# Kernel optimization log

Measured on AMD Instinct MI355X. Metric: run time of the kernel, lower is better.

## Reference

```python
import jax, jax.numpy as jnp
import numpy as np

N = 64
DX = np.pi / N
# torch.fft.fftfreq(N+1, d) == np.fft.fftfreq(N+1) / d ; d varies per env so keep base freqs
BASE_FREQ = (2.0 * np.pi * np.fft.fftfreq(N + 1)).astype(np.float32)  # [65]
DOMAIN = np.array([0.75, 1.0, 0.75, 1.0, 0.75, 1.0, 0.75, 1.0], dtype=np.float32)


def _poisson_solve(w, dx_b):
    # w: [B,N,N] vorticity (already negated), dx_b: [B]
    w_pad = jnp.pad(w, ((0, 0), (0, 1), (0, 1)), mode='wrap')          # circular pad (0,1,0,1) -> [B,65,65]
    wf = jnp.fft.fft2(w_pad / (N ** 2))
    f = BASE_FREQ[None, :] / dx_b[:, None]                             # [B,65] per-env wavenumbers
    k2 = f[:, :, None] ** 2 + f[:, None, :] ** 2                       # [B,65,65] (meshgrid 'ij': kxx^2+kyy^2)
    uf = -wf / (1e-12 + k2)
    uf = uf.at[:, 0, 0].set(0.0)
    return jnp.fft.ifft2((N ** 2) * uf).real[:, :N, :N]                # [B,N,N]


def reference(t, y0, env, params):
    x = y0[:, 0]                                                       # [B,N,N]
    env = env.astype(jnp.int32)
    mu = params[env, 0][:, None, None]                                 # [B,1,1]
    fdx = (jnp.asarray(DOMAIN)[env] * DX)[:, None, None]               # [B,1,1]

    psi = _poisson_solve(-x, fdx[:, 0, 0])

    dxp = lambda a: jnp.roll(a, -1, axis=2) - jnp.roll(a, 1, axis=2)   # derive_x
    dyp = lambda a: jnp.roll(a, -1, axis=1) - jnp.roll(a, 1, axis=1)   # derive_y
    inv4 = 1.0 / (4.0 * fdx ** 2)

    J1 = (dyp(psi) * dxp(x) - dxp(psi) * dyp(x)) * inv4
    J2 = (jnp.roll(x, -1, axis=2) * dyp(jnp.roll(psi, -1, axis=2))
          - jnp.roll(x, 1, axis=2) * dyp(jnp.roll(psi, 1, axis=2))
          - jnp.roll(x, -1, axis=1) * dxp(jnp.roll(psi, -1, axis=1))
          + jnp.roll(x, 1, axis=1) * dxp(jnp.roll(psi, 1, axis=1))) * inv4
    J3 = (jnp.roll(x, (-1, -1), axis=(1, 2)) * (jnp.roll(psi, -1, axis=1) - jnp.roll(psi, -1, axis=2))
          - jnp.roll(x, (1, 1), axis=(1, 2)) * (jnp.roll(psi, 1, axis=2) - jnp.roll(psi, 1, axis=1))
          - jnp.roll(x, (-1, 1), axis=(1, 2)) * (jnp.roll(psi, -1, axis=1) - jnp.roll(psi, 1, axis=2))
          + jnp.roll(x, (1, -1), axis=(1, 2)) * (jnp.roll(psi, -1, axis=2) - jnp.roll(psi, 1, axis=1))) * inv4

    # circular-pad conv2d with kernel [[0,1,0],[1,-4,1],[1,1,0]] == cross-correlation stencil below
    lap = (jnp.roll(x, 1, axis=1) + jnp.roll(x, -1, axis=1)
           + jnp.roll(x, 1, axis=2) + jnp.roll(x, -1, axis=2)
           + jnp.roll(x, (-1, 1), axis=(1, 2)) - 4.0 * x) / (fdx ** 2)

    dudt = -(J1 + J2 + J3) / 3.0 + mu * lap
    return dudt[:, None]                                               # [B,1,N,N]


def setup_inputs() -> dict:
    key = jax.random.key(0)
    k1, k2 = jax.random.split(key)
    B, n_env = 2048, 8
    y0 = jax.random.normal(k1, (B, 1, N, N), dtype=jnp.float32)
    env = jax.random.randint(k2, (B,), 0, n_env, dtype=jnp.int64)
    params = jnp.concatenate([jnp.full((n_env, 1), 0.005, jnp.float32),
                              jnp.full((n_env, 1), 1.0, jnp.float32)], axis=1)
    t = jnp.zeros((1,), dtype=jnp.float32)
    return {"t": t, "y0": y0, "env": env, "params": params}
```

## Files before the change

kernel.cpp:

```cpp
#include <hip/hip_runtime.h>
#include <hip/hip_bf16.h>
#include <math.h>

#define P65 65
#define PLANE_U16 5248
#define SIDE_OFF  5120
#define PSI_U16   8320

__device__ __align__(16) ushort gAfrag[18*512];
__device__ float  g_MpPad[65*68];
__device__ float  g64tab[65];

__device__ __constant__ float c_DOMAIN[8] = {0.75f,1.0f,0.75f,1.0f,0.75f,1.0f,0.75f,1.0f};

__device__ inline ushort f2bf(float f) {
  return __bfloat16_as_ushort(__float2bfloat16(f));
}
__device__ inline float bf2f(ushort h) { return __uint_as_float(((unsigned)h) << 16); }

__device__ inline void barrier_lds() {
  asm volatile("s_waitcnt lgkmcnt(0)" ::: "memory");
  __builtin_amdgcn_sched_barrier(0);
  __builtin_amdgcn_s_barrier();
  __builtin_amdgcn_sched_barrier(0);
}

__device__ inline float Gvalf(int r, int i) {
  int m = (r <= 32) ? r : (r - 32);
  int prod = (m * (i % 65)) % 65;
  float ang = 6.2831853071795864769f * (float)prod / 65.0f;
  return (r <= 32) ? cosf(ang) : sinf(ang);
}
__device__ inline float Gfoldf(int r, int i) {
  float v = Gvalf(r, i);
  if (i == 0) v += Gvalf(r, 64);
  return v;
}

__global__ void init_tables() {
  int tid = blockIdx.x*blockDim.x + threadIdx.x;
  int nth = gridDim.x*blockDim.x;
  for (int idx = tid; idx < 18*512; idx += nth) {
    int blk = idx >> 9, rem = idx & 511;
    int lane = rem >> 3, e = rem & 7;
    int i16 = lane & 15, kg = lane >> 4;
    float v = 0.f;
    if (blk < 10) {
      int mt = blk >> 1, kt = blk & 1;
      int r = 16*mt + i16;
      int i = 32*kt + 8*kg + e;
      if (r < 65 && i < 64) v = Gfoldf(r, i);
    } else {
      int b2 = blk - 10;
      int mt = b2 >> 1, kt = b2 & 1;
      int j  = 16*mt + i16;
      int k1 = 32*kt + 8*kg + e;
      if (j < 64 && k1 < 64) v = Gvalf(k1, j);
    }
    gAfrag[idx] = f2bf(v);
  }
  for (int idx = tid; idx < 65*68; idx += nth) {
    int k2 = idx/68, k1 = idx%68;
    float v = 0.f;
    if (k1 <= 64 && (k1 | k2)) {
      float n1 = (k1==0)?(1.0f/65.0f):(2.0f/65.0f);
      float n2 = (k2==0)?(1.0f/65.0f):(2.0f/65.0f);
      int m1 = (k1<=32)?k1:(k1-32), m2 = (k2<=32)?k2:(k2-32);
      float b1 = 6.2831853071795864769f*(float)m1/65.0f;
      float b2 = 6.2831853071795864769f*(float)m2/65.0f;
      v = (n1*n2)/(b1*b1 + b2*b2);
    }
    g_MpPad[idx] = v;
  }
  for (int idx = tid; idx < 65; idx += nth)
    g64tab[idx] = (idx < 64) ? Gvalf(64, idx) : 0.f;
}

typedef __attribute__((ext_vector_type(8))) short bf16x8;
typedef __attribute__((ext_vector_type(4))) float f32x4;

template<int JT, int TBLOFF>
__device__ inline void prefetchA(bf16x8 (&pre)[2][2], int wvu, int lane, int NTL) {
  #pragma unroll
  for (int tb = 0; tb < 2; ++tb) {
    int tile = wvu + 8*tb;
    int tl = (tile < NTL) ? tile : 0;
    int jt = tl % JT;
    #pragma unroll
    for (int kt = 0; kt < 2; ++kt)
      pre[tb][kt] = *(const bf16x8*)(gAfrag + (TBLOFF + jt*2 + kt)*512 + lane*8);
  }
}

template<int IT, int JT, int TBLOFF, bool SCALE, bool RK, bool PSI>
__device__ inline void stage(const bf16x8 (&pre)[2][2],
                             const ushort* __restrict__ Lin,
                             ushort* __restrict__ Lout,
                             float* __restrict__ psiout,
                             int wvu, int lane)
{
  const int lg = lane >> 4, li = lane & 15;
  constexpr int NTL = IT*JT;
  constexpr int TPW = (NTL + 7) >> 3;
  #pragma unroll
  for (int tb = 0; tb < TPW; ++tb) {
    const int tile = wvu + 8*tb;
    if (tile >= NTL) continue;
    const int it = tile / JT, jt = tile - it*JT;
    f32x4 acc = {0.f, 0.f, 0.f, 0.f};
    #pragma unroll
    for (int kt = 0; kt < 2; ++kt) {
      bf16x8 af = (tb < 2) ? pre[tb][kt]
                           : *(const bf16x8*)(gAfrag + (TBLOFF + jt*2 + kt)*512 + lane*8);
      bf16x8 df = *(const bf16x8*)(Lin + (it*2 + kt)*512 + lane*8);
      acc = __builtin_amdgcn_mfma_f32_16x16x32_bf16(df, af, acc, 0, 0, 0);
    }
    const int f     = 16*jt + li;
    const int dbase = 16*it + 4*lg;
    const bool dEdge = (IT == 5) && (it == IT-1);
    const bool fEdge = (JT == 5) && (jt == JT-1);

    float v[4];
    #pragma unroll
    for (int r = 0; r < 4; ++r) v[r] = acc[r];

    if (SCALE) {
      const float* mp = g_MpPad + (fEdge ? 64 : f)*68 + (dEdge ? 64 : dbase);
      if (dEdge) v[0] *= mp[0];
      else {
        f32x4 m4 = *(const f32x4*)mp;
        #pragma unroll
        for (int r = 0; r < 4; ++r) v[r] *= m4[r];
      }
    }
    if (RK) {
      float gv = g64tab[f];
      uint2 sc = *(const uint2*)(Lin + SIDE_OFF + dbase);
      v[0] = fmaf(bf2f((ushort)(sc.x      )), gv, v[0]);
      v[1] = fmaf(bf2f((ushort)(sc.x >> 16)), gv, v[1]);
      v[2] = fmaf(bf2f((ushort)(sc.y      )), gv, v[2]);
      v[3] = fmaf(bf2f((ushort)(sc.y >> 16)), gv, v[3]);
    }

    if (PSI) {
      #pragma unroll
      for (int r = 0; r < 4; ++r) psiout[f*65 + dbase + r] = v[r];
    } else if (dEdge) {
      if (lg == 0 && (!fEdge || li == 0))
        Lout[SIDE_OFF + f] = f2bf(v[0]);
    } else {
      if (!fEdge || li == 0) {
        int wb = (2*jt + (it>>1))*512 + ((2*it + (lg>>1))&3)*128 + li*8 + 4*(lg&1);
        uint2 pk;
        pk.x = ((unsigned)f2bf(v[1]) << 16) | (unsigned)f2bf(v[0]);
        pk.y = ((unsigned)f2bf(v[3]) << 16) | (unsigned)f2bf(v[2]);
        *(uint2*)(Lout + wb) = pk;
      }
    }
  }
}

__device__ inline float shflx(float v, int srclane) { return __shfl(v, srclane, 64); }

__global__ void __launch_bounds__(512) pde_main(const float* __restrict__ y0,
                                                const int*   __restrict__ env,
                                                const float* __restrict__ params,
                                                float*       __restrict__ out)
{
  __shared__ __align__(16) ushort Lsh[PLANE_U16 + PSI_U16];
  ushort* PB   = Lsh;
  ushort* PA   = Lsh + PLANE_U16;
  float*  Ppsi = (float*)(Lsh + PLANE_U16);

  const int b    = blockIdx.x;
  const int t    = threadIdx.x;
  const int lane = t & 63;
  const int wvu  = __builtin_amdgcn_readfirstlane(t >> 6);

  const int   e       = env[b];
  const float mu      = params[2*e];
  const float fdx     = c_DOMAIN[e] * (float)(3.14159265358979323846/64.0);
  const float inv_dx2 = 1.0f/(fdx*fdx);

  const float* xb = y0 + (size_t)b*4096;

  const int j0 = wvu*8, jm0 = (j0+63)&63, jp8 = (j0+8)&63;
  float xbm = xb[jm0*64 + lane];
  float xbp = xb[jp8*64 + lane];

  float xr[8];
  bf16x8 hv;
  #pragma unroll
  for (int k=0;k<8;++k) {
    float v = xb[(8*wvu + k)*64 + lane];
    xr[k] = v;
    hv[k] = (short)f2bf(v);
  }
  {
    int wb = ((lane>>4)*2 + (wvu>>2))*512 + ((wvu&3)*16 + (lane&15))*8;
    *(bf16x8*)(PA + wb) = hv;
  }
  bf16x8 p1[2][2];  prefetchA<5,0>(p1, wvu, lane, 20);
  barrier_lds();

  stage<4,5, 0,false,false,false>(p1, PA, PB, nullptr, wvu, lane);
  bf16x8 p2[2][2];  prefetchA<5,0>(p2, wvu, lane, 25);
  barrier_lds();

  stage<5,5, 0,true ,false,false>(p2, PB, PA, nullptr, wvu, lane);
  bf16x8 p3[2][2];  prefetchA<4,10>(p3, wvu, lane, 20);
  barrier_lds();

  stage<5,4,10,false,true ,false>(p3, PA, PB, nullptr, wvu, lane);
  bf16x8 p4[2][2];  prefetchA<4,10>(p4, wvu, lane, 16);
  barrier_lds();

  stage<4,4,10,false,true ,true >(p4, PB, nullptr, Ppsi, wvu, lane);
  barrier_lds();

  {
    const int c = lane, cm = (c+63)&63, cp = (c+1)&63;
    const int cB = c*65, cmB = cm*65, cpB = cp*65;
    float* op = out + (size_t)b*4096;

    float xm_c = xbm,   xm_m = shflx(xm_c, cm), xm_p = shflx(xm_c, cp);
    float xc_c = xr[0], xc_m = shflx(xc_c, cm), xc_p = shflx(xc_c, cp);
    float pm_m = Ppsi[cmB+jm0], pm_c = Ppsi[cB+jm0], pm_p = Ppsi[cpB+jm0];
    float pc_m = Ppsi[cmB+j0 ], pc_c = Ppsi[cB+j0 ], pc_p = Ppsi[cpB+j0 ];

    #pragma unroll
    for (int m=0;m<8;++m) {
      int j = j0 + m, jp = (j+1)&63;
      float xn_c = (m < 7) ? xr[m+1] : xbp;
      float xn_m = shflx(xn_c, cm), xn_p = shflx(xn_c, cp);
      float pn_m = Ppsi[cmB+jp], pn_c = Ppsi[cB+jp], pn_p = Ppsi[cpB+jp];

      float J1 = (pn_c - pm_c)*(xc_p - xc_m) - (pc_p - pc_m)*(xn_c - xm_c);
      float J2 = xc_p*(pn_p - pm_p) - xc_m*(pn_m - pm_m)
               - xn_c*(pn_p - pn_m) + xm_c*(pm_p - pm_m);
      float J3 = xn_p*(pn_c - pc_p) - xm_m*(pc_m - pm_c)
               - xn_m*(pn_c - pc_m) + xm_p*(pc_p - pm_c);
      float lap = (xm_c + xn_c + xc_m + xc_p + xn_m - 4.0f*xc_c) * inv_dx2;

      op[j*64 + c] = -(J1 + J2 + J3)*(0.25f/3.0f) + mu*lap;

      xm_m=xc_m; xm_c=xc_c; xm_p=xc_p;  pm_m=pc_m; pm_c=pc_c; pm_p=pc_p;
      xc_m=xn_m; xc_c=xn_c; xc_p=xn_p;  pc_m=pn_m; pc_c=pn_c; pc_p=pn_p;
    }
  }
}

extern "C" void kernel_launch(void* const* d_in, const int* in_sizes, int n_in,
                              void* d_out, int out_size, void* d_ws, size_t ws_size,
                              hipStream_t stream) {
  const float* y0     = (const float*)d_in[1];
  const int*   env    = (const int*)  d_in[2];
  const float* params = (const float*)d_in[3];
  float*       out    = (float*)d_out;
  int B = in_sizes[1] / 4096;

  init_tables<<<64, 256, 0, stream>>>();
  pde_main<<<B, 512, 0, stream>>>(y0, env, params, out);
}
```

Before: 34.54 us.

## Process two images per block, sharing prefetched DFT fragments across both

Each workgroup now handles two batch images instead of one, with LDS doubled to hold both planes. The prefetched A-matrix fragments for each transform stage are reused for both images, and each stage is issued twice per barrier, halving the number of blocks and barriers per image. The cost is double the LDS and more register pressure per block, which may lower occupancy, and half as many blocks to spread across CUs.

```diff
diff --git a/kernel.cpp b/kernel.cpp
--- a/kernel.cpp
+++ b/kernel.cpp
@@ -6,6 +6,7 @@
 #define PLANE_U16 5248
 #define SIDE_OFF  5120
 #define PSI_U16   8320
+#define IMG_U16   (PLANE_U16 + PSI_U16)
 
 __device__ __align__(16) ushort gAfrag[18*512];
 __device__ float  g_MpPad[65*68];
@@ -162,92 +163,118 @@
 
 __device__ inline float shflx(float v, int srclane) { return __shfl(v, srclane, 64); }
 
+__device__ inline void stencil_img(const float* __restrict__ Ppsi,
+                                   const float* __restrict__ xr,
+                                   float xbm, float xbp,
+                                   float mu, float id2,
+                                   float* __restrict__ op,
+                                   int wvu, int lane, bool store)
+{
+  const int c = lane, cm = (c+63)&63, cp = (c+1)&63;
+  const int cB = c*65, cmB = cm*65, cpB = cp*65;
+  const int j0 = wvu*8, jm0 = (j0+63)&63;
+
+  float xm_c = xbm,   xm_m = shflx(xm_c, cm), xm_p = shflx(xm_c, cp);
+  float xc_c = xr[0], xc_m = shflx(xc_c, cm), xc_p = shflx(xc_c, cp);
+  float pm_m = Ppsi[cmB+jm0], pm_c = Ppsi[cB+jm0], pm_p = Ppsi[cpB+jm0];
+  float pc_m = Ppsi[cmB+j0 ], pc_c = Ppsi[cB+j0 ], pc_p = Ppsi[cpB+j0 ];
+
+  #pragma unroll
+  for (int m=0;m<8;++m) {
+    int j = j0 + m, jp = (j+1)&63;
+    float xn_c = (m < 7) ? xr[m+1] : xbp;
+    float xn_m = shflx(xn_c, cm), xn_p = shflx(xn_c, cp);
+    float pn_m = Ppsi[cmB+jp], pn_c = Ppsi[cB+jp], pn_p = Ppsi[cpB+jp];
+
+    float J1 = (pn_c - pm_c)*(xc_p - xc_m) - (pc_p - pc_m)*(xn_c - xm_c);
+    float J2 = xc_p*(pn_p - pm_p) - xc_m*(pn_m - pm_m)
+             - xn_c*(pn_p - pn_m) + xm_c*(pm_p - pm_m);
+    float J3 = xn_p*(pn_c - pc_p) - xm_m*(pc_m - pm_c)
+             - xn_m*(pn_c - pc_m) + xm_p*(pc_p - pm_c);
+    float lap = (xm_c + xn_c + xc_m + xc_p + xn_m - 4.0f*xc_c) * id2;
+
+    if (store) op[j*64 + c] = -(J1 + J2 + J3)*(0.25f/3.0f) + mu*lap;
+
+    xm_m=xc_m; xm_c=xc_c; xm_p=xc_p;  pm_m=pc_m; pm_c=pc_c; pm_p=pc_p;
+    xc_m=xn_m; xc_c=xn_c; xc_p=xn_p;  pc_m=pn_m; pc_c=pn_c; pc_p=pn_p;
+  }
+}
+
 __global__ void __launch_bounds__(512) pde_main(const float* __restrict__ y0,
                                                 const int*   __restrict__ env,
                                                 const float* __restrict__ params,
-                                                float*       __restrict__ out)
+                                                float*       __restrict__ out,
+                                                int B)
 {
-  __shared__ __align__(16) ushort Lsh[PLANE_U16 + PSI_U16];
-  ushort* PB   = Lsh;
-  ushort* PA   = Lsh + PLANE_U16;
-  float*  Ppsi = (float*)(Lsh + PLANE_U16);
-
-  const int b    = blockIdx.x;
+  __shared__ __align__(16) ushort Lsh[2*IMG_U16];
+  ushort* PB0 = Lsh;
+  ushort* PA0 = Lsh + PLANE_U16;
+  float*  Ps0 = (float*)(Lsh + PLANE_U16);
+  ushort* PB1 = Lsh + IMG_U16;
+  ushort* PA1 = Lsh + IMG_U16 + PLANE_U16;
+  float*  Ps1 = (float*)(Lsh + IMG_U16 + PLANE_U16);
+
   const int t    = threadIdx.x;
   const int lane = t & 63;
   const int wvu  = __builtin_amdgcn_readfirstlane(t >> 6);
 
-  const int   e       = env[b];
-  const float mu      = params[2*e];
-  const float fdx     = c_DOMAIN[e] * (float)(3.14159265358979323846/64.0);
-  const float inv_dx2 = 1.0f/(fdx*fdx);
-
-  const float* xb = y0 + (size_t)b*4096;
+  const int b0  = 2*blockIdx.x;
+  const int b1r = b0 + 1;
+  const bool has2 = (b1r < B);
+  const int b1 = has2 ? b1r : b0;
+
+  const int   e0 = env[b0], e1 = env[b1];
+  const float mu0 = params[2*e0], mu1 = params[2*e1];
+  const float fdx0 = c_DOMAIN[e0] * (float)(3.14159265358979323846/64.0);
+  const float fdx1 = c_DOMAIN[e1] * (float)(3.14159265358979323846/64.0);
+  const float id20 = 1.0f/(fdx0*fdx0);
+  const float id21 = 1.0f/(fdx1*fdx1);
+
+  const float* xb0 = y0 + (size_t)b0*4096;
+  const float* xb1 = y0 + (size_t)b1*4096;
 
   const int j0 = wvu*8, jm0 = (j0+63)&63, jp8 = (j0+8)&63;
-  float xbm = xb[jm0*64 + lane];
-  float xbp = xb[jp8*64 + lane];
-
-  float xr[8];
-  bf16x8 hv;
-  #pragma unroll
-  for (int k=0;k<8;++k) {
-    float v = xb[(8*wvu + k)*64 + lane];
-    xr[k] = v;
-    hv[k] = (short)f2bf(v);
-  }
+  float xbm0 = xb0[jm0*64 + lane], xbp0 = xb0[jp8*64 + lane];
+  float xbm1 = xb1[jm0*64 + lane], xbp1 = xb1[jp8*64 + lane];
+
+  float xr0[8], xr1[8];
   {
+    bf16x8 h0, h1;
+    #pragma unroll
+    for (int k=0;k<8;++k) {
+      float v0 = xb0[(8*wvu + k)*64 + lane];
+      float v1 = xb1[(8*wvu + k)*64 + lane];
+      xr0[k] = v0;  h0[k] = (short)f2bf(v0);
+      xr1[k] = v1;  h1[k] = (short)f2bf(v1);
+    }
     int wb = ((lane>>4)*2 + (wvu>>2))*512 + ((wvu&3)*16 + (lane&15))*8;
-    *(bf16x8*)(PA + wb) = hv;
+    *(bf16x8*)(PA0 + wb) = h0;
+    *(bf16x8*)(PA1 + wb) = h1;
   }
   bf16x8 p1[2][2];  prefetchA<5,0>(p1, wvu, lane, 20);
   barrier_lds();
 
-  stage<4,5, 0,false,false,false>(p1, PA, PB, nullptr, wvu, lane);
+  stage<4,5, 0,false,false,false>(p1, PA0, PB0, nullptr, wvu, lane);
+  stage<4,5, 0,false,false,false>(p1, PA1, PB1, nullptr, wvu, lane);
   bf16x8 p2[2][2];  prefetchA<5,0>(p2, wvu, lane, 25);
   barrier_lds();
 
-  stage<5,5, 0,true ,false,false>(p2, PB, PA, nullptr, wvu, lane);
+  stage<5,5, 0,true ,false,false>(p2, PB0, PA0, nullptr, wvu, lane);
+  stage<5,5, 0,true ,false,false>(p2, PB1, PA1, nullptr, wvu, lane);
   bf16x8 p3[2][2];  prefetchA<4,10>(p3, wvu, lane, 20);
   barrier_lds();
 
-  stage<5,4,10,false,true ,false>(p3, PA, PB, nullptr, wvu, lane);
+  stage<5,4,10,false,true ,false>(p3, PA0, PB0, nullptr, wvu, lane);
+  stage<5,4,10,false,true ,false>(p3, PA1, PB1, nullptr, wvu, lane);
   bf16x8 p4[2][2];  prefetchA<4,10>(p4, wvu, lane, 16);
   barrier_lds();
 
-  stage<4,4,10,false,true ,true >(p4, PB, nullptr, Ppsi, wvu, lane);
-  barrier_lds();
-
-  {
-    const int c = lane, cm = (c+63)&63, cp = (c+1)&63;
-    const int cB = c*65, cmB = cm*65, cpB = cp*65;
-    float* op = out + (size_t)b*4096;
-
-    float xm_c = xbm,   xm_m = shflx(xm_c, cm), xm_p = shflx(xm_c, cp);
-    float xc_c = xr[0], xc_m = shflx(xc_c, cm), xc_p = shflx(xc_c, cp);
-    float pm_m = Ppsi[cmB+jm0], pm_c = Ppsi[cB+jm0], pm_p = Ppsi[cpB+jm0];
-    float pc_m = Ppsi[cmB+j0 ], pc_c = Ppsi[cB+j0 ], pc_p = Ppsi[cpB+j0 ];
-
-    #pragma unroll
-    for (int m=0;m<8;++m) {
-      int j = j0 + m, jp = (j+1)&63;
-      float xn_c = (m < 7) ? xr[m+1] : xbp;
-      float xn_m = shflx(xn_c, cm), xn_p = shflx(xn_c, cp);
-      float pn_m = Ppsi[cmB+jp], pn_c = Ppsi[cB+jp], pn_p = Ppsi[cpB+jp];
-
-      float J1 = (pn_c - pm_c)*(xc_p - xc_m) - (pc_p - pc_m)*(xn_c - xm_c);
-      float J2 = xc_p*(pn_p - pm_p) - xc_m*(pn_m - pm_m)
-               - xn_c*(pn_p - pn_m) + xm_c*(pm_p - pm_m);
-      float J3 = xn_p*(pn_c - pc_p) - xm_m*(pc_m - pm_c)
-               - xn_m*(pn_c - pc_m) + xm_p*(pc_p - pm_c);
-      float lap = (xm_c + xn_c + xc_m + xc_p + xn_m - 4.0f*xc_c) * inv_dx2;
-
-      op[j*64 + c] = -(J1 + J2 + J3)*(0.25f/3.0f) + mu*lap;
-
-      xm_m=xc_m; xm_c=xc_c; xm_p=xc_p;  pm_m=pc_m; pm_c=pc_c; pm_p=pc_p;
-      xc_m=xn_m; xc_c=xn_c; xc_p=xn_p;  pc_m=pn_m; pc_c=pn_c; pc_p=pn_p;
-    }
-  }
+  stage<4,4,10,false,true ,true >(p4, PB0, nullptr, Ps0, wvu, lane);
+  stage<4,4,10,false,true ,true >(p4, PB1, nullptr, Ps1, wvu, lane);
+  barrier_lds();
+
+  stencil_img(Ps0, xr0, xbm0, xbp0, mu0, id20, out + (size_t)b0*4096, wvu, lane, true);
+  stencil_img(Ps1, xr1, xbm1, xbp1, mu1, id21, out + (size_t)b1*4096, wvu, lane, has2);
 }
 
 extern "C" void kernel_launch(void* const* d_in, const int* in_sizes, int n_in,
@@ -258,7 +285,8 @@
   const float* params = (const float*)d_in[3];
   float*       out    = (float*)d_out;
   int B = in_sizes[1] / 4096;
+  int nb = (B + 1) / 2;
 
   init_tables<<<64, 256, 0, stream>>>();
-  pde_main<<<B, 512, 0, stream>>>(y0, env, params, out);
-}
+  pde_main<<<nb, 512, 0, stream>>>(y0, env, params, out, B);
+}
```

Measured after the change: 38.99 us. 12.9% more time.
